# Kernel optimization log

Hardware: AMD Instinct MI355X
Metric: run time of the kernel (lower is better)

The kernel has to match this reference:

```python
import jax, jax.numpy as jnp
import numpy as np

N = 2097152
RES = 512
N_LEVELS = 6  # 512,256,128,64,32,16 (stop at LIGHT_MIN_RES=16)
MIN_ROUGHNESS = 0.08
MAX_ROUGHNESS = 0.5


def _dot(a, b):
    return jnp.sum(a * b, axis=-1, keepdims=True)


def _safe_normalize(x):
    return x / jnp.sqrt(jnp.clip(_dot(x, x), 1e-20, None))


def _reflect(x, n):
    return 2.0 * _dot(x, n) * n - x


def _rgb_to_srgb(x):
    return jnp.where(x <= 0.0031308, 12.92 * x,
                     1.055 * jnp.power(jnp.maximum(x, 0.0031308), 1.0 / 2.4) - 0.055)


def _cube_face_uv(d):
    # OpenGL / nvdiffrast cube-map convention (inverse of util.cube_to_dir)
    x, y, z = d[..., 0], d[..., 1], d[..., 2]
    ax, ay, az = jnp.abs(x), jnp.abs(y), jnp.abs(z)
    is_x = (ax >= ay) & (ax >= az)
    is_y = (~is_x) & (ay >= az)
    face = jnp.where(is_x, jnp.where(x > 0, 0, 1),
           jnp.where(is_y, jnp.where(y > 0, 2, 3),
                           jnp.where(z > 0, 4, 5)))
    ma = jnp.maximum(jnp.where(is_x, ax, jnp.where(is_y, ay, az)), 1e-20)
    u = jnp.where(is_x, jnp.where(x > 0, -z, z),
        jnp.where(is_y, x, jnp.where(z > 0, x, -x)))
    v = jnp.where(is_y, jnp.where(y > 0, z, -z), -y)
    return face, u / ma, v / ma


def _bilinear_gather(tex, face, fx, fy):
    # tex: [6,H,W,C]; face/fx/fy: [N]
    H, W = tex.shape[1], tex.shape[2]
    x0 = jnp.floor(fx); y0 = jnp.floor(fy)
    tx = (fx - x0)[:, None]; ty = (fy - y0)[:, None]
    x0i = jnp.clip(x0.astype(jnp.int32), 0, W - 1)
    x1i = jnp.clip(x0i + 1, 0, W - 1)
    y0i = jnp.clip(y0.astype(jnp.int32), 0, H - 1)
    y1i = jnp.clip(y0i + 1, 0, H - 1)
    c00 = tex[face, y0i, x0i]; c01 = tex[face, y0i, x1i]
    c10 = tex[face, y1i, x0i]; c11 = tex[face, y1i, x1i]
    return (c00 * (1 - tx) + c01 * tx) * (1 - ty) + (c10 * (1 - tx) + c11 * tx) * ty


def _sample_cubemap(tex, dirs):
    H, W = tex.shape[1], tex.shape[2]
    face, u, v = _cube_face_uv(dirs)
    return _bilinear_gather(tex, face, (u * 0.5 + 0.5) * W - 0.5, (v * 0.5 + 0.5) * H - 0.5)


def _sample_cubemap_mip(mips, dirs, level):
    # trilinear: bilinear in each of the two bracketing mip levels + lerp on level
    L = len(mips)
    samples = jnp.stack([_sample_cubemap(m, dirs) for m in mips], axis=0)  # [L,N,C]
    lvl = jnp.clip(level, 0.0, L - 1.0)
    l0 = jnp.floor(lvl).astype(jnp.int32)
    l1 = jnp.minimum(l0 + 1, L - 1)
    f = (lvl - l0.astype(lvl.dtype))[:, None]
    n = jnp.arange(dirs.shape[0])
    return samples[l0, n] * (1 - f) + samples[l1, n] * f


def _sample_lut(lut, uv):
    # lut: [H,W,C]; uv in [0,1], u -> width, v -> height, clamp boundary
    H, W = lut.shape[0], lut.shape[1]
    fx = uv[:, 0] * W - 0.5; fy = uv[:, 1] * H - 0.5
    x0 = jnp.floor(fx); y0 = jnp.floor(fy)
    tx = (fx - x0)[:, None]; ty = (fy - y0)[:, None]
    x0i = jnp.clip(x0.astype(jnp.int32), 0, W - 1); x1i = jnp.clip(x0i + 1, 0, W - 1)
    y0i = jnp.clip(y0.astype(jnp.int32), 0, H - 1); y1i = jnp.clip(y0i + 1, 0, H - 1)
    c00 = lut[y0i, x0i]; c01 = lut[y0i, x1i]; c10 = lut[y1i, x0i]; c11 = lut[y1i, x1i]
    return (c00 * (1 - tx) + c01 * tx) * (1 - ty) + (c10 * (1 - tx) + c11 * tx) * ty


def _get_mip(roughness, n_levels):
    lo = (jnp.clip(roughness, MIN_ROUGHNESS, MAX_ROUGHNESS) - MIN_ROUGHNESS) \
         / (MAX_ROUGHNESS - MIN_ROUGHNESS) * (n_levels - 2)
    hi = (jnp.clip(roughness, MAX_ROUGHNESS, 1.0) - MAX_ROUGHNESS) / (1.0 - MAX_ROUGHNESS) + n_levels - 2
    return jnp.where(roughness < MAX_ROUGHNESS, lo, hi)


def _shade(view_dir, normal, kd, ks, reflect_occ, diffuse_map, mips, fg_lut):
    roughness = ks[:, 1:2]
    metallic = ks[:, 2:3]
    spec_col = (1.0 - metallic) * 0.04 + kd * metallic
    diff_col = kd * (1.0 - metallic)
    reflvec = _safe_normalize(_reflect(view_dir, normal))
    diffuse = jnp.clip(_sample_cubemap(diffuse_map, normal), 0.0, None)
    shaded = diffuse * diff_col * (1.0 - ks[:, 0:1])
    NdotV = jnp.clip(_dot(view_dir, normal), 1e-4, None)
    fg = _sample_lut(fg_lut, jnp.concatenate([NdotV, roughness], axis=-1))
    miplevel = _get_mip(roughness[:, 0], len(mips))
    spec = jnp.clip(_sample_cubemap_mip(mips, reflvec, miplevel), 0.0, None)
    reflectance = spec_col * fg[:, 0:1] + fg[:, 1:2]
    shaded = shaded + spec * reflectance * (1.0 - reflect_occ)
    return _rgb_to_srgb(jnp.clip(shaded, 0.0, 1.0))


def setup_inputs() -> dict:
    key = jax.random.key(0)
    k = jax.random.split(key, 16)
    inp = {
        "view_dir": _safe_normalize(jax.random.normal(k[0], (N, 3), jnp.float32)),
        "normal": _safe_normalize(jax.random.normal(k[1], (N, 3), jnp.float32)),
        "kd": jax.random.uniform(k[2], (N, 3), jnp.float32),
        "ks": jax.random.uniform(k[3], (N, 3), jnp.float32),
        "reflect_occ": jax.random.uniform(k[4], (N, 1), jnp.float32),
    }
    # learned / prefiltered environment light parameters (from build_mips)
    inp["diffuse_map"] = jax.random.uniform(k[5], (6, 16, 16, 3), jnp.float32)
    res = RES
    for i in range(N_LEVELS):
        inp[f"spec{i}"] = jax.random.uniform(k[6 + i], (6, res, res, 3), jnp.float32)
        res //= 2
    inp["fg_lut"] = jax.random.uniform(k[12], (256, 256, 2), jnp.float32)
    return inp


def reference(view_dir, normal, kd, ks, reflect_occ, diffuse_map,
              spec0, spec1, spec2, spec3, spec4, spec5, fg_lut):
    mips = [spec0, spec1, spec2, spec3, spec4, spec5]
    return _shade(view_dir, normal, kd, ks, reflect_occ, diffuse_map, mips, fg_lut)
```

## Files before the change

### kernel.cpp

```cpp
#include <hip/hip_runtime.h>
#include <hip/hip_fp16.h>
#include <math.h>


typedef unsigned int u32;

__device__ __forceinline__ u32 enc9e5(float r, float g, float b) {
    r = fminf(fmaxf(r, 0.f), 65408.f);
    g = fminf(fmaxf(g, 0.f), 65408.f);
    b = fminf(fmaxf(b, 0.f), 65408.f);
    float maxc = fmaxf(r, fmaxf(g, b));
    int e = ((__float_as_int(maxc) >> 23) & 0xff) - 127;
    int exp_p = max(e + 16, 0);
    float rd = __int_as_float((151 - exp_p) << 23);
    int maxm = (int)(maxc * rd + 0.5f);
    if (maxm == 512) { exp_p += 1; rd *= 0.5f; }
    u32 rm = (u32)(r * rd + 0.5f);
    u32 gm = (u32)(g * rd + 0.5f);
    u32 bm = (u32)(b * rd + 0.5f);
    return rm | (gm << 9) | (bm << 18) | ((u32)exp_p << 27);
}

__device__ __forceinline__ void dec9e5_acc(u32 pk, float w, float& r, float& g, float& b) {
    float scale = __int_as_float((int)(((pk >> 27) & 31u) + 103u) << 23) * w;
    r += (float)(pk & 511u) * scale;
    g += (float)((pk >> 9) & 511u) * scale;
    b += (float)((pk >> 18) & 511u) * scale;
}

__device__ __forceinline__ void gather_q9(uint4 q, float tx, float ty,
                                          float& r, float& g, float& b) {
    float w00 = (1.f - tx) * (1.f - ty);
    float w01 = tx * (1.f - ty);
    float w10 = (1.f - tx) * ty;
    float w11 = tx * ty;
    r = 0.f; g = 0.f; b = 0.f;
    dec9e5_acc(q.x, w00, r, g, b);
    dec9e5_acc(q.y, w01, r, g, b);
    dec9e5_acc(q.z, w10, r, g, b);
    dec9e5_acc(q.w, w11, r, g, b);
}

__device__ __forceinline__ float srgb1(float x) {
    float p = 1.055f * __builtin_amdgcn_exp2f(
                  __builtin_amdgcn_logf(fmaxf(x, 0.0031308f)) * (1.0f / 2.4f)) - 0.055f;
    return (x <= 0.0031308f) ? (12.92f * x) : p;
}

__device__ __forceinline__ void cube_face_uv(float dx, float dy, float dz,
                                             int& face, float& u, float& v) {
    float ax = fabsf(dx), ay = fabsf(dy), az = fabsf(dz);
    bool is_x = (ax >= ay) && (ax >= az);
    bool is_y = (!is_x) && (ay >= az);
    face = is_x ? (dx > 0.f ? 0 : 1)
                : (is_y ? (dy > 0.f ? 2 : 3) : (dz > 0.f ? 4 : 5));
    float ma = fmaxf(is_x ? ax : (is_y ? ay : az), 1e-20f);
    float uu = is_x ? (dx > 0.f ? -dz : dz) : (is_y ? dx : (dz > 0.f ? dx : -dx));
    float vv = is_y ? (dy > 0.f ? dz : -dz) : -dy;
    float inv = __builtin_amdgcn_rcpf(ma);
    u = uu * inv;
    v = vv * inv;
}

#define SPEC_TOTAL 2096640
#define DIF_OFF    SPEC_TOTAL
#define LUT_OFF    (SPEC_TOTAL + 1536)
#define ALL_QUADS  (SPEC_TOTAL + 1536 + 65536)
#define N_TILES    8452

__device__ __forceinline__ int spec_off(int l) {
    return (1 << 21) - ((1 << 21) >> (2 * l));
}

__global__ __launch_bounds__(256)
void repack_tiled(const float* __restrict__ s0, const float* __restrict__ s1,
                  const float* __restrict__ s2, const float* __restrict__ s3,
                  const float* __restrict__ s4, const float* __restrict__ s5,
                  const float* __restrict__ diffuse_map,
                  const float2* __restrict__ lut,
                  uint4* __restrict__ dst)
{
    __shared__ u32 L[289];
    int b = blockIdx.x;
    int tid = threadIdx.x;

    if (b >= 8196) {
        int t = b - 8196;
        int ty0 = (t >> 4) << 4;
        int tx0 = (t & 15) << 4;
        for (int e = tid; e < 289; e += 256) {
            int ey = e / 17, ex = e - ey * 17;
            int gy = min(ty0 + ey, 255), gx = min(tx0 + ex, 255);
            float2 c = lut[(gy << 8) + gx];
            __half2 h = __floats2half2_rn(c.x, c.y);
            L[e] = *reinterpret_cast<u32*>(&h);
        }
        __syncthreads();
        int qx = tid & 15, qy = tid >> 4;
        uint4 qv;
        qv.x = L[qy * 17 + qx];       qv.y = L[qy * 17 + qx + 1];
        qv.z = L[(qy + 1) * 17 + qx]; qv.w = L[(qy + 1) * 17 + qx + 1];
        dst[LUT_OFF + ((ty0 + qy) << 8) + tx0 + qx] = qv;
        return;
    }

    const float* src; int lr, tbase, doff;
    if      (b < 6144) { src = s0; lr = 9; tbase = 0;    doff = 0; }
    else if (b < 7680) { src = s1; lr = 8; tbase = 6144; doff = 1572864; }
    else if (b < 8064) { src = s2; lr = 7; tbase = 7680; doff = 1966080; }
    else if (b < 8160) { src = s3; lr = 6; tbase = 8064; doff = 2064384; }
    else if (b < 8184) { src = s4; lr = 5; tbase = 8160; doff = 2088960; }
    else if (b < 8190) { src = s5; lr = 4; tbase = 8184; doff = 2095104; }
    else               { src = diffuse_map; lr = 4; tbase = 8190; doff = DIF_OFF; }

    int W = 1 << lr;
    int lt = lr - 4;
    int local = b - tbase;
    int face = local >> (2 * lt);
    int rem  = local & ((1 << (2 * lt)) - 1);
    int ty0 = (rem >> lt) << 4;
    int tx0 = (rem & ((1 << lt) - 1)) << 4;
    int fbase = face << (2 * lr);

    for (int e = tid; e < 289; e += 256) {
        int ey = e / 17, ex = e - ey * 17;
        int gy = min(ty0 + ey, W - 1), gx = min(tx0 + ex, W - 1);
        int idx = 3 * (fbase + (gy << lr) + gx);
        L[e] = enc9e5(src[idx], src[idx + 1], src[idx + 2]);
    }
    __syncthreads();
    int qx = tid & 15, qy = tid >> 4;
    uint4 qv;
    qv.x = L[qy * 17 + qx];       qv.y = L[qy * 17 + qx + 1];
    qv.z = L[(qy + 1) * 17 + qx]; qv.w = L[(qy + 1) * 17 + qx + 1];
    dst[doff + fbase + ((ty0 + qy) << lr) + tx0 + qx] = qv;
}


struct Frac {
    float dtx, dty, ltx, lty, atx, aty, btx, bty, fmip;
};

__device__ __forceinline__ void prep_pt2(const float* s, int t, const uint4* __restrict__ q,
                                         Frac& p, uint4& qA, uint4& qB, uint4& ql, uint4& qd) {
    float vx = s[3 * t],        vy = s[3 * t + 1],        vz = s[3 * t + 2];
    float nx = s[1536 + 3 * t], ny = s[1536 + 3 * t + 1], nz = s[1536 + 3 * t + 2];
    float rough = s[4608 + 3 * t + 1];

    float vdotn = vx * nx + vy * ny + vz * nz;
    float rx = 2.f * vdotn * nx - vx;
    float ry = 2.f * vdotn * ny - vy;
    float rz = 2.f * vdotn * nz - vz;
    float rinv = __builtin_amdgcn_rsqf(fmaxf(rx * rx + ry * ry + rz * rz, 1e-20f));
    rx *= rinv; ry *= rinv; rz *= rinv;

    int dI;
    {
        int face; float u, v;
        cube_face_uv(nx, ny, nz, face, u, v);
        float fx = (u * 0.5f + 0.5f) * 16.f - 0.5f;
        float fy = (v * 0.5f + 0.5f) * 16.f - 0.5f;
        float x0f = floorf(fx), y0f = floorf(fy);
        p.dtx = fx - x0f; p.dty = fy - y0f;
        int x0 = min(max((int)x0f, 0), 15);
        int y0 = min(max((int)y0f, 0), 15);
        dI = DIF_OFF + (face << 8) + (y0 << 4) + x0;
    }

    int lI;
    {
        float NdotV = fmaxf(vdotn, 1e-4f);
        float fx = NdotV * 256.f - 0.5f;
        float fy = rough * 256.f - 0.5f;
        float x0f = floorf(fx), y0f = floorf(fy);
        p.ltx = fx - x0f; p.lty = fy - y0f;
        int x0 = min(max((int)x0f, 0), 255);
        int y0 = min(max((int)y0f, 0), 255);
        lI = LUT_OFF + (y0 << 8) + x0;
    }

    const float MINR = 0.08f, MAXR = 0.5f;
    float lo = (fminf(fmaxf(rough, MINR), MAXR) - MINR) * (4.0f / (MAXR - MINR));
    float hi = (fminf(fmaxf(rough, MAXR), 1.0f) - MAXR) * (1.0f / (1.0f - MAXR)) + 4.0f;
    float lvl = fminf(fmaxf((rough < MAXR) ? lo : hi, 0.f), 5.f);
    int l0 = min(max((int)floorf(lvl), 0), 5);
    int l1 = min(l0 + 1, 5);
    p.fmip = lvl - (float)l0;

    int aI, bI;
    {
        int face; float u, v;
        cube_face_uv(rx, ry, rz, face, u, v);
        int lrA = 9 - l0, lrB = 9 - l1;
        float RA = (float)(1 << lrA);
        float fxA = (u * 0.5f + 0.5f) * RA - 0.5f;
        float fyA = (v * 0.5f + 0.5f) * RA - 0.5f;
        float fxB = (l0 == l1) ? fxA : (fxA + 0.5f) * 0.5f - 0.5f;
        float fyB = (l0 == l1) ? fyA : (fyA + 0.5f) * 0.5f - 0.5f;

        float x0fA = floorf(fxA), y0fA = floorf(fyA);
        p.atx = fxA - x0fA; p.aty = fyA - y0fA;
        int WA = 1 << lrA;
        int x0A = min(max((int)x0fA, 0), WA - 1);
        int y0A = min(max((int)y0fA, 0), WA - 1);
        aI = spec_off(l0) + (face << (2 * lrA)) + (y0A << lrA) + x0A;

        float x0fB = floorf(fxB), y0fB = floorf(fyB);
        p.btx = fxB - x0fB; p.bty = fyB - y0fB;
        int WB = 1 << lrB;
        int x0B = min(max((int)x0fB, 0), WB - 1);
        int y0B = min(max((int)y0fB, 0), WB - 1);
        bI = spec_off(l1) + (face << (2 * lrB)) + (y0B << lrB) + x0B;
    }

    qA = q[aI];
    qB = q[bI];
    ql = q[lI];
    qd = q[dI];
}

__device__ __forceinline__ void finish_pt2(float* s, int t, const Frac& p,
                                           uint4 qA, uint4 qB, uint4 ql, uint4 qd) {
    float kdx = s[3072 + 3 * t], kdy = s[3072 + 3 * t + 1], kdz = s[3072 + 3 * t + 2];
    float ks0 = s[4608 + 3 * t];
    float met = s[4608 + 3 * t + 2];
    float occ = s[6144 + t];

    float ar, ag, ab_, br, bg, bb;
    gather_q9(qA, p.atx, p.aty, ar, ag, ab_);
    gather_q9(qB, p.btx, p.bty, br, bg, bb);

    __half2 h00 = *reinterpret_cast<__half2*>(&ql.x);
    __half2 h01 = *reinterpret_cast<__half2*>(&ql.y);
    __half2 h10 = *reinterpret_cast<__half2*>(&ql.z);
    __half2 h11 = *reinterpret_cast<__half2*>(&ql.w);
    float2 c00 = __half22float2(h00), c01 = __half22float2(h01);
    float2 c10 = __half22float2(h10), c11 = __half22float2(h11);
    float lw00 = (1.f - p.ltx) * (1.f - p.lty);
    float lw01 = p.ltx * (1.f - p.lty);
    float lw10 = (1.f - p.ltx) * p.lty;
    float lw11 = p.ltx * p.lty;
    float fg0 = c00.x * lw00 + c01.x * lw01 + c10.x * lw10 + c11.x * lw11;
    float fg1 = c00.y * lw00 + c01.y * lw01 + c10.y * lw10 + c11.y * lw11;

    float dfr, dfg, dfb;
    gather_q9(qd, p.dtx, p.dty, dfr, dfg, dfb);
    dfr = fmaxf(dfr, 0.f); dfg = fmaxf(dfg, 0.f); dfb = fmaxf(dfb, 0.f);

    float spr = fmaxf(ar * (1.f - p.fmip) + br * p.fmip, 0.f);
    float spg = fmaxf(ag * (1.f - p.fmip) + bg * p.fmip, 0.f);
    float spb = fmaxf(ab_ * (1.f - p.fmip) + bb * p.fmip, 0.f);

    float m = met;
    float scx = (1.f - m) * 0.04f + kdx * m;
    float scy = (1.f - m) * 0.04f + kdy * m;
    float scz = (1.f - m) * 0.04f + kdz * m;
    float dcx = kdx * (1.f - m);
    float dcy = kdy * (1.f - m);
    float dcz = kdz * (1.f - m);

    float kds = 1.f - ks0;
    float om = 1.f - occ;
    float shx = dfr * dcx * kds + spr * (scx * fg0 + fg1) * om;
    float shy = dfg * dcy * kds + spg * (scy * fg0 + fg1) * om;
    float shz = dfb * dcz * kds + spb * (scz * fg0 + fg1) * om;

    s[3 * t + 0] = srgb1(fminf(fmaxf(shx, 0.f), 1.f));
    s[3 * t + 1] = srgb1(fminf(fmaxf(shy, 0.f), 1.f));
    s[3 * t + 2] = srgb1(fminf(fmaxf(shz, 0.f), 1.f));
}

__global__ __launch_bounds__(256, 6)
void envlight_p2(const float* __restrict__ view_dir,
                 const float* __restrict__ normal,
                 const float* __restrict__ kd,
                 const float* __restrict__ ks,
                 const float* __restrict__ reflect_occ,
                 const uint4* __restrict__ q,
                 float* __restrict__ out, int n)
{
    __shared__ float s_in[6656];
    int tid = threadIdx.x;
    int base = blockIdx.x << 9;
    int nblk = min(512, n - base);

    if (nblk == 512) {
        const float4* v4 = (const float4*)(view_dir + 3 * base);
        const float4* n4 = (const float4*)(normal + 3 * base);
        const float4* k4 = (const float4*)(kd + 3 * base);
        const float4* q4 = (const float4*)(ks + 3 * base);
        const float4* o4 = (const float4*)(reflect_occ + base);
        float4* dst4 = (float4*)s_in;
        #pragma unroll
        for (int k = 0; k < 7; ++k) {
            int j = tid + (k << 8);
            if (j < 1664) {
                const float4* src; int off;
                if (j < 384)       { src = v4; off = j; }
                else if (j < 768)  { src = n4; off = j - 384; }
                else if (j < 1152) { src = k4; off = j - 768; }
                else if (j < 1536) { src = q4; off = j - 1152; }
                else               { src = o4; off = j - 1536; }
                dst4[j] = src[off];
            }
        }
    } else {
        for (int j = tid; j < nblk * 3; j += 256) {
            s_in[j]        = view_dir[3 * base + j];
            s_in[1536 + j] = normal[3 * base + j];
            s_in[3072 + j] = kd[3 * base + j];
            s_in[4608 + j] = ks[3 * base + j];
        }
        for (int j = tid; j < nblk; j += 256)
            s_in[6144 + j] = reflect_occ[base + j];
    }
    __syncthreads();

    bool a0 = (tid < nblk);
    bool a1 = (tid + 256 < nblk);

    Frac f0, f1;
    uint4 qA0, qB0, ql0, qd0, qA1, qB1, ql1, qd1;

    if (a0) prep_pt2(s_in, tid,       q, f0, qA0, qB0, ql0, qd0);
    if (a1) prep_pt2(s_in, tid + 256, q, f1, qA1, qB1, ql1, qd1);
    if (a0) finish_pt2(s_in, tid,       f0, qA0, qB0, ql0, qd0);
    if (a1) finish_pt2(s_in, tid + 256, f1, qA1, qB1, ql1, qd1);

    __syncthreads();

    if (nblk == 512) {
        float4* ot4 = (float4*)(out + 3 * base);
        #pragma unroll
        for (int k = 0; k < 2; ++k) {
            int j = tid + (k << 8);
            if (j < 384) ot4[j] = ((const float4*)s_in)[j];
        }
    } else {
        for (int j = tid; j < nblk * 3; j += 256)
            out[3 * base + j] = s_in[j];
    }
}

__global__ __launch_bounds__(256)
void envlight_raw(const float* __restrict__ view_dir,
                  const float* __restrict__ normal,
                  const float* __restrict__ kd,
                  const float* __restrict__ ks,
                  const float* __restrict__ reflect_occ,
                  const float* __restrict__ diffuse_map,
                  const float* __restrict__ s0, const float* __restrict__ s1,
                  const float* __restrict__ s2, const float* __restrict__ s3,
                  const float* __restrict__ s4, const float* __restrict__ s5,
                  const float* __restrict__ fg_lut,
                  float* __restrict__ out, int n)
{
    int i = blockIdx.x * blockDim.x + threadIdx.x;
    if (i >= n) return;

    float vx = view_dir[3 * i], vy = view_dir[3 * i + 1], vz = view_dir[3 * i + 2];
    float nx = normal[3 * i],  ny = normal[3 * i + 1],  nz = normal[3 * i + 2];
    float kdx = kd[3 * i], kdy = kd[3 * i + 1], kdz = kd[3 * i + 2];
    float ks0 = ks[3 * i], rough = ks[3 * i + 1], metallic = ks[3 * i + 2];
    float occ = reflect_occ[i];

    float vdotn = vx * nx + vy * ny + vz * nz;
    float rx = 2.f * vdotn * nx - vx;
    float ry = 2.f * vdotn * ny - vy;
    float rz = 2.f * vdotn * nz - vz;
    float rinv = __builtin_amdgcn_rsqf(fmaxf(rx * rx + ry * ry + rz * rz, 1e-20f));
    rx *= rinv; ry *= rinv; rz *= rinv;

    const float* mips[6] = {s0, s1, s2, s3, s4, s5};

    const float MINR = 0.08f, MAXR = 0.5f;
    float lo = (fminf(fmaxf(rough, MINR), MAXR) - MINR) * (4.0f / (MAXR - MINR));
    float hi = (fminf(fmaxf(rough, MAXR), 1.0f) - MAXR) * (1.0f / (1.0f - MAXR)) + 4.0f;
    float lvl = fminf(fmaxf((rough < MAXR) ? lo : hi, 0.f), 5.f);
    int l0 = min(max((int)floorf(lvl), 0), 5);
    int l1 = min(l0 + 1, 5);
    float f = lvl - (float)l0;

    float acc[3][3];
    float dirs[3][3] = {{nx, ny, nz}, {rx, ry, rz}, {rx, ry, rz}};
    int lrs[3] = {4, 9 - l0, 9 - l1};
    const float* texs[3] = {diffuse_map, mips[l0], mips[l1]};
    for (int s = 0; s < 3; ++s) {
        int face; float u, v;
        cube_face_uv(dirs[s][0], dirs[s][1], dirs[s][2], face, u, v);
        int lr = lrs[s], W = 1 << lr;
        float fx = (u * 0.5f + 0.5f) * (float)W - 0.5f;
        float fy = (v * 0.5f + 0.5f) * (float)W - 0.5f;
        float x0f = floorf(fx), y0f = floorf(fy);
        float tx = fx - x0f, ty = fy - y0f;
        int x0 = min(max((int)x0f, 0), W - 1);
        int x1 = min(x0 + 1, W - 1);
        int y0 = min(max((int)y0f, 0), W - 1);
        int y1 = min(y0 + 1, W - 1);
        int base = face << (2 * lr);
        const float* t = texs[s];
        const float* p00 = t + 3 * (base + (y0 << lr) + x0);
        const float* p01 = t + 3 * (base + (y0 << lr) + x1);
        const float* p10 = t + 3 * (base + (y1 << lr) + x0);
        const float* p11 = t + 3 * (base + (y1 << lr) + x1);
        float w00 = (1.f - tx) * (1.f - ty), w01 = tx * (1.f - ty);
        float w10 = (1.f - tx) * ty, w11 = tx * ty;
        for (int c = 0; c < 3; ++c)
            acc[s][c] = p00[c] * w00 + p01[c] * w01 + p10[c] * w10 + p11[c] * w11;
    }

    float NdotV = fmaxf(vdotn, 1e-4f);
    float fx = NdotV * 256.f - 0.5f, fy = rough * 256.f - 0.5f;
    float x0f = floorf(fx), y0f = floorf(fy);
    float tx = fx - x0f, ty = fy - y0f;
    int x0 = min(max((int)x0f, 0), 255);
    int x1 = min(x0 + 1, 255);
    int y0 = min(max((int)y0f, 0), 255);
    int y1 = min(y0 + 1, 255);
    const float2* lut2 = (const float2*)fg_lut;
    float2 c00 = lut2[(y0 << 8) + x0], c01 = lut2[(y0 << 8) + x1];
    float2 c10 = lut2[(y1 << 8) + x0], c11 = lut2[(y1 << 8) + x1];
    float w00 = (1.f - tx) * (1.f - ty), w01 = tx * (1.f - ty);
    float w10 = (1.f - tx) * ty, w11 = tx * ty;
    float fg0 = c00.x * w00 + c01.x * w01 + c10.x * w10 + c11.x * w11;
    float fg1 = c00.y * w00 + c01.y * w01 + c10.y * w10 + c11.y * w11;

    float dfr = fmaxf(acc[0][0], 0.f), dfg = fmaxf(acc[0][1], 0.f), dfb = fmaxf(acc[0][2], 0.f);
    float spr = fmaxf(acc[1][0] * (1.f - f) + acc[2][0] * f, 0.f);
    float spg = fmaxf(acc[1][1] * (1.f - f) + acc[2][1] * f, 0.f);
    float spb = fmaxf(acc[1][2] * (1.f - f) + acc[2][2] * f, 0.f);

    float m = metallic;
    float scx = (1.f - m) * 0.04f + kdx * m;
    float scy = (1.f - m) * 0.04f + kdy * m;
    float scz = (1.f - m) * 0.04f + kdz * m;
    float kds = 1.f - ks0;
    float om = 1.f - occ;
    float shx = dfr * kdx * (1.f - m) * kds + spr * (scx * fg0 + fg1) * om;
    float shy = dfg * kdy * (1.f - m) * kds + spg * (scy * fg0 + fg1) * om;
    float shz = dfb * kdz * (1.f - m) * kds + spb * (scz * fg0 + fg1) * om;

    out[3 * i + 0] = srgb1(fminf(fmaxf(shx, 0.f), 1.f));
    out[3 * i + 1] = srgb1(fminf(fmaxf(shy, 0.f), 1.f));
    out[3 * i + 2] = srgb1(fminf(fmaxf(shz, 0.f), 1.f));
}

extern "C" void kernel_launch(void* const* d_in, const int* in_sizes, int n_in,
                              void* d_out, int out_size, void* d_ws, size_t ws_size,
                              hipStream_t stream) {
    const float* view_dir    = (const float*)d_in[0];
    const float* normal      = (const float*)d_in[1];
    const float* kd          = (const float*)d_in[2];
    const float* ks          = (const float*)d_in[3];
    const float* reflect_occ = (const float*)d_in[4];
    const float* diffuse_map = (const float*)d_in[5];
    const float* s0          = (const float*)d_in[6];
    const float* s1          = (const float*)d_in[7];
    const float* s2          = (const float*)d_in[8];
    const float* s3          = (const float*)d_in[9];
    const float* s4          = (const float*)d_in[10];
    const float* s5          = (const float*)d_in[11];
    const float* fg_lut      = (const float*)d_in[12];
    float* out = (float*)d_out;

    int n = in_sizes[0] / 3;
    const size_t NEED_Q = (size_t)ALL_QUADS * 16;

    if (ws_size >= NEED_Q) {
        uint4* q = (uint4*)d_ws;
        repack_tiled<<<N_TILES, 256, 0, stream>>>(
            s0, s1, s2, s3, s4, s5, diffuse_map, (const float2*)fg_lut, q);
        int grid = (n + 511) / 512;
        envlight_p2<<<grid, 256, 0, stream>>>(
            view_dir, normal, kd, ks, reflect_occ, q, out, n);
    } else {
        int grid = (n + 255) / 256;
        envlight_raw<<<grid, 256, 0, stream>>>(
            view_dir, normal, kd, ks, reflect_occ, diffuse_map,
            s0, s1, s2, s3, s4, s5, fg_lut, out, n);
    }
}
```

Before: 242.1 us.

## Pipeline input staging with double-buffered async LDS loads in persistent blocks

Replaces the one-shot 512-point-per-block shading kernel with a persistent grid of up to 2048 blocks. Each block walks 256-point chunks and stages the next chunk's inputs into a second LDS buffer with global_load_lds while it shades the current chunk. Each thread now shades one point and writes its three output floats directly to global memory instead of going back through LDS. The aim is to hide input-load latency behind the texture-gather work. In exchange the output stores are less coalesced, each thread has less overlap across independent points, and correctness depends on the async LDS loads completing before the barrier.

```diff
diff --git a/kernel.cpp b/kernel.cpp
--- a/kernel.cpp
+++ b/kernel.cpp
@@ -67,9 +67,17 @@
 #define LUT_OFF    (SPEC_TOTAL + 1536)
 #define ALL_QUADS  (SPEC_TOTAL + 1536 + 65536)
 #define N_TILES    8452
+#define MAIN_GRID  2048
 
 __device__ __forceinline__ int spec_off(int l) {
     return (1 << 21) - ((1 << 21) >> (2 * l));
+}
+
+__device__ __forceinline__ void gld16(const float4* g, float4* l) {
+    __builtin_amdgcn_global_load_lds(
+        (const __attribute__((address_space(1))) void*)g,
+        (__attribute__((address_space(3))) void*)l,
+        16, 0, 0);
 }
 
 __global__ __launch_bounds__(256)
@@ -136,16 +144,52 @@
     dst[doff + fbase + ((ty0 + qy) << lr) + tx0 + qx] = qv;
 }
 
-
-struct Frac {
-    float dtx, dty, ltx, lty, atx, aty, btx, bty, fmip;
-};
-
-__device__ __forceinline__ void prep_pt2(const float* s, int t, const uint4* __restrict__ q,
-                                         Frac& p, uint4& qA, uint4& qB, uint4& ql, uint4& qd) {
-    float vx = s[3 * t],        vy = s[3 * t + 1],        vz = s[3 * t + 2];
-    float nx = s[1536 + 3 * t], ny = s[1536 + 3 * t + 1], nz = s[1536 + 3 * t + 2];
-    float rough = s[4608 + 3 * t + 1];
+__device__ __forceinline__ void stage_chunk(float* sb, int tid,
+    const float* __restrict__ vd, const float* __restrict__ nm,
+    const float* __restrict__ kd, const float* __restrict__ ks,
+    const float* __restrict__ oc, int base, int nblk)
+{
+    if (nblk == 256) {
+        const float4* v4 = (const float4*)(vd + 3 * base);
+        const float4* n4 = (const float4*)(nm + 3 * base);
+        const float4* k4 = (const float4*)(kd + 3 * base);
+        const float4* q4 = (const float4*)(ks + 3 * base);
+        const float4* o4 = (const float4*)(oc + base);
+        float4* d4 = (float4*)sb;
+        #pragma unroll
+        for (int kk = 0; kk < 4; ++kk) {
+            int j = tid + (kk << 8);
+            if (j < 832) {
+                const float4* src; int off;
+                if (j < 192)      { src = v4; off = j; }
+                else if (j < 384) { src = n4; off = j - 192; }
+                else if (j < 576) { src = k4; off = j - 384; }
+                else if (j < 768) { src = q4; off = j - 576; }
+                else              { src = o4; off = j - 768; }
+                gld16(src + off, d4 + j);
+            }
+        }
+    } else {
+        for (int j = tid; j < nblk * 3; j += 256) {
+            sb[j]        = vd[3 * base + j];
+            sb[768 + j]  = nm[3 * base + j];
+            sb[1536 + j] = kd[3 * base + j];
+            sb[2304 + j] = ks[3 * base + j];
+        }
+        for (int j = tid; j < nblk; j += 256)
+            sb[3072 + j] = oc[base + j];
+    }
+}
+
+__device__ __forceinline__ void shade_pt(const float* s, int tid,
+                                         const uint4* __restrict__ q,
+                                         float* __restrict__ outp)
+{
+    float vx = s[3 * tid], vy = s[3 * tid + 1], vz = s[3 * tid + 2];
+    float nx = s[768 + 3 * tid], ny = s[768 + 3 * tid + 1], nz = s[768 + 3 * tid + 2];
+    float kdx = s[1536 + 3 * tid], kdy = s[1536 + 3 * tid + 1], kdz = s[1536 + 3 * tid + 2];
+    float ks0 = s[2304 + 3 * tid], rough = s[2304 + 3 * tid + 1], metallic = s[2304 + 3 * tid + 2];
+    float occ = s[3072 + tid];
 
     float vdotn = vx * nx + vy * ny + vz * nz;
     float rx = 2.f * vdotn * nx - vx;
@@ -154,29 +198,29 @@
     float rinv = __builtin_amdgcn_rsqf(fmaxf(rx * rx + ry * ry + rz * rz, 1e-20f));
     rx *= rinv; ry *= rinv; rz *= rinv;
 
-    int dI;
+    float dtx, dty; int dIdx;
     {
         int face; float u, v;
         cube_face_uv(nx, ny, nz, face, u, v);
         float fx = (u * 0.5f + 0.5f) * 16.f - 0.5f;
         float fy = (v * 0.5f + 0.5f) * 16.f - 0.5f;
         float x0f = floorf(fx), y0f = floorf(fy);
-        p.dtx = fx - x0f; p.dty = fy - y0f;
+        dtx = fx - x0f; dty = fy - y0f;
         int x0 = min(max((int)x0f, 0), 15);
         int y0 = min(max((int)y0f, 0), 15);
-        dI = DIF_OFF + (face << 8) + (y0 << 4) + x0;
-    }
-
-    int lI;
+        dIdx = (face << 8) + (y0 << 4) + x0;
+    }
+
+    float ltx, lty; int lutI;
     {
         float NdotV = fmaxf(vdotn, 1e-4f);
         float fx = NdotV * 256.f - 0.5f;
         float fy = rough * 256.f - 0.5f;
         float x0f = floorf(fx), y0f = floorf(fy);
-        p.ltx = fx - x0f; p.lty = fy - y0f;
+        ltx = fx - x0f; lty = fy - y0f;
         int x0 = min(max((int)x0f, 0), 255);
         int y0 = min(max((int)y0f, 0), 255);
-        lI = LUT_OFF + (y0 << 8) + x0;
+        lutI = (y0 << 8) + x0;
     }
 
     const float MINR = 0.08f, MAXR = 0.5f;
@@ -185,9 +229,9 @@
     float lvl = fminf(fmaxf((rough < MAXR) ? lo : hi, 0.f), 5.f);
     int l0 = min(max((int)floorf(lvl), 0), 5);
     int l1 = min(l0 + 1, 5);
-    p.fmip = lvl - (float)l0;
-
-    int aI, bI;
+    float fmip = lvl - (float)l0;
+
+    float atx, aty, btx, bty; int aIdx, bIdx;
     {
         int face; float u, v;
         cube_face_uv(rx, ry, rz, face, u, v);
@@ -199,59 +243,51 @@
         float fyB = (l0 == l1) ? fyA : (fyA + 0.5f) * 0.5f - 0.5f;
 
         float x0fA = floorf(fxA), y0fA = floorf(fyA);
-        p.atx = fxA - x0fA; p.aty = fyA - y0fA;
+        atx = fxA - x0fA; aty = fyA - y0fA;
         int WA = 1 << lrA;
         int x0A = min(max((int)x0fA, 0), WA - 1);
         int y0A = min(max((int)y0fA, 0), WA - 1);
-        aI = spec_off(l0) + (face << (2 * lrA)) + (y0A << lrA) + x0A;
+        aIdx = spec_off(l0) + (face << (2 * lrA)) + (y0A << lrA) + x0A;
 
         float x0fB = floorf(fxB), y0fB = floorf(fyB);
-        p.btx = fxB - x0fB; p.bty = fyB - y0fB;
+        btx = fxB - x0fB; bty = fyB - y0fB;
         int WB = 1 << lrB;
         int x0B = min(max((int)x0fB, 0), WB - 1);
         int y0B = min(max((int)y0fB, 0), WB - 1);
-        bI = spec_off(l1) + (face << (2 * lrB)) + (y0B << lrB) + x0B;
-    }
-
-    qA = q[aI];
-    qB = q[bI];
-    ql = q[lI];
-    qd = q[dI];
-}
-
-__device__ __forceinline__ void finish_pt2(float* s, int t, const Frac& p,
-                                           uint4 qA, uint4 qB, uint4 ql, uint4 qd) {
-    float kdx = s[3072 + 3 * t], kdy = s[3072 + 3 * t + 1], kdz = s[3072 + 3 * t + 2];
-    float ks0 = s[4608 + 3 * t];
-    float met = s[4608 + 3 * t + 2];
-    float occ = s[6144 + t];
+        bIdx = spec_off(l1) + (face << (2 * lrB)) + (y0B << lrB) + x0B;
+    }
+
+    uint4 qA = q[aIdx];
+    uint4 qB = q[bIdx];
+    uint4 lq = (q + LUT_OFF)[lutI];
+    uint4 dq = (q + DIF_OFF)[dIdx];
 
     float ar, ag, ab_, br, bg, bb;
-    gather_q9(qA, p.atx, p.aty, ar, ag, ab_);
-    gather_q9(qB, p.btx, p.bty, br, bg, bb);
-
-    __half2 h00 = *reinterpret_cast<__half2*>(&ql.x);
-    __half2 h01 = *reinterpret_cast<__half2*>(&ql.y);
-    __half2 h10 = *reinterpret_cast<__half2*>(&ql.z);
-    __half2 h11 = *reinterpret_cast<__half2*>(&ql.w);
+    gather_q9(qA, atx, aty, ar, ag, ab_);
+    gather_q9(qB, btx, bty, br, bg, bb);
+
+    __half2 h00 = *reinterpret_cast<__half2*>(&lq.x);
+    __half2 h01 = *reinterpret_cast<__half2*>(&lq.y);
+    __half2 h10 = *reinterpret_cast<__half2*>(&lq.z);
+    __half2 h11 = *reinterpret_cast<__half2*>(&lq.w);
     float2 c00 = __half22float2(h00), c01 = __half22float2(h01);
     float2 c10 = __half22float2(h10), c11 = __half22float2(h11);
-    float lw00 = (1.f - p.ltx) * (1.f - p.lty);
-    float lw01 = p.ltx * (1.f - p.lty);
-    float lw10 = (1.f - p.ltx) * p.lty;
-    float lw11 = p.ltx * p.lty;
+    float lw00 = (1.f - ltx) * (1.f - lty);
+    float lw01 = ltx * (1.f - lty);
+    float lw10 = (1.f - ltx) * lty;
+    float lw11 = ltx * lty;
     float fg0 = c00.x * lw00 + c01.x * lw01 + c10.x * lw10 + c11.x * lw11;
     float fg1 = c00.y * lw00 + c01.y * lw01 + c10.y * lw10 + c11.y * lw11;
 
     float dfr, dfg, dfb;
-    gather_q9(qd, p.dtx, p.dty, dfr, dfg, dfb);
+    gather_q9(dq, dtx, dty, dfr, dfg, dfb);
     dfr = fmaxf(dfr, 0.f); dfg = fmaxf(dfg, 0.f); dfb = fmaxf(dfb, 0.f);
 
-    float spr = fmaxf(ar * (1.f - p.fmip) + br * p.fmip, 0.f);
-    float spg = fmaxf(ag * (1.f - p.fmip) + bg * p.fmip, 0.f);
-    float spb = fmaxf(ab_ * (1.f - p.fmip) + bb * p.fmip, 0.f);
-
-    float m = met;
+    float spr = fmaxf(ar * (1.f - fmip) + br * fmip, 0.f);
+    float spg = fmaxf(ag * (1.f - fmip) + bg * fmip, 0.f);
+    float spb = fmaxf(ab_ * (1.f - fmip) + bb * fmip, 0.f);
+
+    float m = metallic;
     float scx = (1.f - m) * 0.04f + kdx * m;
     float scy = (1.f - m) * 0.04f + kdy * m;
     float scz = (1.f - m) * 0.04f + kdz * m;
@@ -265,80 +301,43 @@
     float shy = dfg * dcy * kds + spg * (scy * fg0 + fg1) * om;
     float shz = dfb * dcz * kds + spb * (scz * fg0 + fg1) * om;
 
-    s[3 * t + 0] = srgb1(fminf(fmaxf(shx, 0.f), 1.f));
-    s[3 * t + 1] = srgb1(fminf(fmaxf(shy, 0.f), 1.f));
-    s[3 * t + 2] = srgb1(fminf(fmaxf(shz, 0.f), 1.f));
+    outp[0] = srgb1(fminf(fmaxf(shx, 0.f), 1.f));
+    outp[1] = srgb1(fminf(fmaxf(shy, 0.f), 1.f));
+    outp[2] = srgb1(fminf(fmaxf(shz, 0.f), 1.f));
 }
 
 __global__ __launch_bounds__(256, 6)
-void envlight_p2(const float* __restrict__ view_dir,
-                 const float* __restrict__ normal,
-                 const float* __restrict__ kd,
-                 const float* __restrict__ ks,
-                 const float* __restrict__ reflect_occ,
-                 const uint4* __restrict__ q,
-                 float* __restrict__ out, int n)
+void envlight_pipe(const float* __restrict__ view_dir,
+                   const float* __restrict__ normal,
+                   const float* __restrict__ kd,
+                   const float* __restrict__ ks,
+                   const float* __restrict__ reflect_occ,
+                   const uint4* __restrict__ q,
+                   float* __restrict__ out, int n)
 {
-    __shared__ float s_in[6656];
+    __shared__ float s_in[2][3328];
     int tid = threadIdx.x;
-    int base = blockIdx.x << 9;
-    int nblk = min(512, n - base);
-
-    if (nblk == 512) {
-        const float4* v4 = (const float4*)(view_dir + 3 * base);
-        const float4* n4 = (const float4*)(normal + 3 * base);
-        const float4* k4 = (const float4*)(kd + 3 * base);
-        const float4* q4 = (const float4*)(ks + 3 * base);
-        const float4* o4 = (const float4*)(reflect_occ + base);
-        float4* dst4 = (float4*)s_in;
-        #pragma unroll
-        for (int k = 0; k < 7; ++k) {
-            int j = tid + (k << 8);
-            if (j < 1664) {
-                const float4* src; int off;
-                if (j < 384)       { src = v4; off = j; }
-                else if (j < 768)  { src = n4; off = j - 384; }
-                else if (j < 1152) { src = k4; off = j - 768; }
-                else if (j < 1536) { src = q4; off = j - 1152; }
-                else               { src = o4; off = j - 1536; }
-                dst4[j] = src[off];
-            }
-        }
-    } else {
-        for (int j = tid; j < nblk * 3; j += 256) {
-            s_in[j]        = view_dir[3 * base + j];
-            s_in[1536 + j] = normal[3 * base + j];
-            s_in[3072 + j] = kd[3 * base + j];
-            s_in[4608 + j] = ks[3 * base + j];
-        }
-        for (int j = tid; j < nblk; j += 256)
-            s_in[6144 + j] = reflect_occ[base + j];
-    }
-    __syncthreads();
-
-    bool a0 = (tid < nblk);
-    bool a1 = (tid + 256 < nblk);
-
-    Frac f0, f1;
-    uint4 qA0, qB0, ql0, qd0, qA1, qB1, ql1, qd1;
-
-    if (a0) prep_pt2(s_in, tid,       q, f0, qA0, qB0, ql0, qd0);
-    if (a1) prep_pt2(s_in, tid + 256, q, f1, qA1, qB1, ql1, qd1);
-    if (a0) finish_pt2(s_in, tid,       f0, qA0, qB0, ql0, qd0);
-    if (a1) finish_pt2(s_in, tid + 256, f1, qA1, qB1, ql1, qd1);
-
-    __syncthreads();
-
-    if (nblk == 512) {
-        float4* ot4 = (float4*)(out + 3 * base);
-        #pragma unroll
-        for (int k = 0; k < 2; ++k) {
-            int j = tid + (k << 8);
-            if (j < 384) ot4[j] = ((const float4*)s_in)[j];
-        }
-    } else {
-        for (int j = tid; j < nblk * 3; j += 256)
-            out[3 * base + j] = s_in[j];
+    int nchunks = (n + 255) >> 8;
+    int c = blockIdx.x;
+    if (c >= nchunks) return;
+
+    stage_chunk(s_in[0], tid, view_dir, normal, kd, ks, reflect_occ,
+                c << 8, min(256, n - (c << 8)));
+
+    int t = 0;
+    for (; c < nchunks; c += gridDim.x, ++t) {
+        int cur = t & 1;
+        __syncthreads();
+
+        int cn = c + gridDim.x;
+        if (cn < nchunks)
+            stage_chunk(s_in[cur ^ 1], tid, view_dir, normal, kd, ks, reflect_occ,
+                        cn << 8, min(256, n - (cn << 8)));
+
+        int base = c << 8;
+        int nblk = min(256, n - base);
+        if (tid < nblk)
+            shade_pt(s_in[cur], tid, q, out + 3 * (base + tid));
     }
 }
 
@@ -470,8 +469,9 @@
         uint4* q = (uint4*)d_ws;
         repack_tiled<<<N_TILES, 256, 0, stream>>>(
             s0, s1, s2, s3, s4, s5, diffuse_map, (const float2*)fg_lut, q);
-        int grid = (n + 511) / 512;
-        envlight_p2<<<grid, 256, 0, stream>>>(
+        int nchunks = (n + 255) >> 8;
+        int grid = min(nchunks, MAIN_GRID);
+        envlight_pipe<<<grid, 256, 0, stream>>>(
             view_dir, normal, kd, ks, reflect_occ, q, out, n);
     } else {
         int grid = (n + 255) / 256;
```

After: 228.9 us. 5.5% less time.
